# Kernel optimization log

Hardware: AMD Instinct MI355X
Metric: run time of the kernel (lower is better)

The kernel has to match this reference:

```python
import jax, jax.numpy as jnp
import numpy as np

N_HEADS = 16
D_MODEL = 1024
NEG_INF = float('-inf')


def _rope_tables(seq_len, d_k, dtype):
    # RoPE(dim=d_k//2): Theta_i = 10000^(-i/dim), repeat-interleaved to width d_k;
    # positions start at 1 (torch uses arange(1, max_len+1)).
    dim = d_k // 2
    theta = jnp.exp(-jnp.arange(dim, dtype=dtype) * (np.log(10000.0) / dim))
    theta = jnp.repeat(theta, 2)                      # [d_k]
    pos = jnp.arange(1, seq_len + 1, dtype=dtype)[:, None]  # [S,1]
    ang = pos * theta                                 # [S,d_k]
    return jnp.sin(ang), jnp.cos(ang)


def _rope(x):
    # x: [B,H,S,d_k]; pair rotation (x0,x1)->(-x1,x0), Rx = x*cos + rot(x)*sin
    B, H, S, d_k = x.shape
    sin, cos = _rope_tables(S, d_k, x.dtype)
    xp = x.reshape(B, H, S, d_k // 2, 2)
    rot = jnp.stack([-xp[..., 1], xp[..., 0]], axis=-1).reshape(x.shape)
    return x * cos + rot * sin


def setup_inputs() -> dict:
    key = jax.random.key(0)
    ks = jax.random.split(key, 8)
    B, S, D, H = 2, 1024, D_MODEL, N_HEADS
    source_query = jax.random.normal(ks[0], (B, S, D), dtype=jnp.float32)
    source_key_value = jax.random.normal(ks[1], (B, S, D), dtype=jnp.float32)
    # tail padding: lengths in [820, 1024]
    q_len = jax.random.randint(ks[2], (B,), 820, S + 1)
    kv_len = jax.random.randint(ks[3], (B,), 820, S + 1)
    pos = jnp.arange(S)
    source_query_padding_mask = pos[None, :] >= q_len[:, None]    # True = pad
    source_key_value_padding_mask = pos[None, :] >= kv_len[:, None]
    prev = jax.random.normal(ks[4], (1, B, H, S, S), dtype=jnp.float32) * 0.5
    Wq = jax.random.normal(ks[5], (D, D), dtype=jnp.float32) * 0.02
    Wk = jax.random.normal(ks[6], (D, D), dtype=jnp.float32) * 0.02
    kv2 = jax.random.split(ks[7], 2)
    Wv = jax.random.normal(kv2[0], (D, D), dtype=jnp.float32) * 0.02
    Wproj = jax.random.normal(kv2[1], (D, D), dtype=jnp.float32) * 0.02
    return dict(source_query=source_query, source_key_value=source_key_value,
                source_query_padding_mask=source_query_padding_mask,
                source_key_value_padding_mask=source_key_value_padding_mask,
                prev=prev, Wq=Wq, Wk=Wk, Wv=Wv, Wproj=Wproj)


def reference(source_query, source_key_value, source_query_padding_mask,
              source_key_value_padding_mask, prev, Wq, Wk, Wv, Wproj):
    B, Sq, D = source_query.shape
    Sk = source_key_value.shape[1]
    H = N_HEADS
    d_k = D // H

    def split_heads(x, S):
        return x.reshape(B, S, H, d_k).transpose(0, 2, 1, 3)  # [B,H,S,d_k]

    # nn.Linear(bias=False): y = x @ W.T
    q = split_heads(jnp.einsum('bsd,ed->bse', source_query, Wq), Sq)
    k = split_heads(jnp.einsum('bsd,ed->bse', source_key_value, Wk), Sk)
    v = split_heads(jnp.einsum('bsd,ed->bse', source_key_value, Wv), Sk)

    q = _rope(q)
    k = _rope(k)

    scores = jnp.einsum('bhqd,bhkd->bhqk', q, k) * (d_k ** -0.5)
    q_pad = source_query_padding_mask[:, None, :, None]   # [B,1,Sq,1]
    kv_pad = source_key_value_padding_mask[:, None, None, :]  # [B,1,1,Sk]
    scores = jnp.where(q_pad, NEG_INF, scores)
    scores = jnp.where(kv_pad, NEG_INF, scores)
    causal = jnp.tril(jnp.ones((Sq, Sq), dtype=bool))      # masked=True
    scores = jnp.where(causal, scores, NEG_INF)

    prev_new = jnp.concatenate([prev, scores[None]], axis=0)  # [L+1,B,H,Sq,Sk]
    avg = prev_new.mean(0)

    # rows fully -inf (padded queries) would softmax to NaN in torch, then get
    # filled with 0 -> compute a safe softmax and zero those rows instead.
    safe = jnp.where(q_pad, 0.0, avg)
    w = jax.nn.softmax(safe, axis=-1)
    w = jnp.where(q_pad, 0.0, w)

    attn = jnp.einsum('bhqk,bhkd->bhqd', w, v)
    attn = attn.transpose(0, 2, 1, 3).reshape(B, Sq, D)
    out = jnp.einsum('bsd,ed->bse', attn, Wproj)  # dropout=0 (eval)
    return out, prev_new
```

## Files before the change

kernel.cpp:

```cpp
#include <hip/hip_runtime.h>
#include <math.h>

#define NSEQ 1024
#define NH   16
#define DKH  64

#define NEGBIG (-1.0e30f)

__global__ __launch_bounds__(256) void normalize_masks(
    const unsigned char* __restrict__ qm, const unsigned char* __restrict__ km,
    int* __restrict__ outq, int* __restrict__ outk)
{
    __shared__ int flag;
    if (threadIdx.x == 0) flag = 0;
    __syncthreads();
    int f = 0;
    for (int i = threadIdx.x; i < 2048; i += 256) {
        if ((i & 3) && qm[i]) f = 1;
        if ((i & 3) && km[i]) f = 1;
    }
    if (f) atomicOr(&flag, 1);
    __syncthreads();
    const int isbyte = flag;
    for (int i = threadIdx.x; i < 2048; i += 256) {
        outq[i] = isbyte ? (int)qm[i] : ((const int*)qm)[i];
        outk[i] = isbyte ? (int)km[i] : ((const int*)km)[i];
    }
}

__device__ __forceinline__ void gemm_core(
    const float* __restrict__ X, const float* __restrict__ W,
    float (*As)[68], float (*Bs)[132], float (&acc)[8][4],
    int m0, int e0, int tid)
{
    const int tm = tid >> 5, tn = tid & 31;
    const int arow = tid >> 2, akq = (tid & 3) * 4;
    const int brow = tid >> 1, bkq = (tid & 1) * 8;
    const float* aptr = &X[(size_t)(m0 + arow) * 1024 + akq];
    const float* bptr = &W[(size_t)(e0 + brow) * 1024 + bkq];

    float4 ar  = *(const float4*)aptr;
    float4 br0 = *(const float4*)bptr;
    float4 br1 = *(const float4*)(bptr + 4);

    for (int k0 = 0; k0 < 1024; k0 += 16) {
        As[akq + 0][arow] = ar.x;  As[akq + 1][arow] = ar.y;
        As[akq + 2][arow] = ar.z;  As[akq + 3][arow] = ar.w;
        Bs[bkq + 0][brow] = br0.x; Bs[bkq + 1][brow] = br0.y;
        Bs[bkq + 2][brow] = br0.z; Bs[bkq + 3][brow] = br0.w;
        Bs[bkq + 4][brow] = br1.x; Bs[bkq + 5][brow] = br1.y;
        Bs[bkq + 6][brow] = br1.z; Bs[bkq + 7][brow] = br1.w;
        __syncthreads();
        if (k0 + 16 < 1024) {
            ar  = *(const float4*)(aptr + k0 + 16);
            br0 = *(const float4*)(bptr + k0 + 16);
            br1 = *(const float4*)(bptr + k0 + 16 + 4);
        }
        #pragma unroll
        for (int k = 0; k < 16; ++k) {
            float a[8], bb[4];
            *(float4*)&a[0]  = *(const float4*)&As[k][tm * 8];
            *(float4*)&a[4]  = *(const float4*)&As[k][tm * 8 + 4];
            *(float4*)&bb[0] = *(const float4*)&Bs[k][tn * 4];
            #pragma unroll
            for (int i = 0; i < 8; ++i)
                #pragma unroll
                for (int j = 0; j < 4; ++j)
                    acc[i][j] += a[i] * bb[j];
        }
        __syncthreads();
    }
}

__global__ __launch_bounds__(256) void gemm_qkv(
    const float* __restrict__ srcq, const float* __restrict__ srckv,
    const float* __restrict__ Wq, const float* __restrict__ Wk,
    const float* __restrict__ Wv,
    float* __restrict__ qh, float* __restrict__ kh, float* __restrict__ vh)
{
    __shared__ float As[16][68];
    __shared__ float Bs[16][132];
    const int tid = threadIdx.x;
    const int z = blockIdx.z;
    const float* X = (z == 0) ? srcq : srckv;
    const float* W = (z == 0) ? Wq : (z == 1) ? Wk : Wv;
    float* Y       = (z == 0) ? qh : (z == 1) ? kh : vh;
    const int m0 = blockIdx.y * 64, e0 = blockIdx.x * 128;

    float acc[8][4] = {{0.f}};
    gemm_core(X, W, As, Bs, acc, m0, e0, tid);

    const int tm = tid >> 5, tn = tid & 31;
    const int col = e0 + tn * 4;
    const int h = col >> 6, dbase = col & 63;
    const bool rope = (z != 2);
    float th0 = 0.f, th1 = 0.f;
    if (rope) {
        const float cth = 0.28782313662425575f;
        th0 = expf(-(float)(dbase >> 1) * cth);
        th1 = expf(-(float)((dbase >> 1) + 1) * cth);
    }
    #pragma unroll
    for (int i = 0; i < 8; ++i) {
        const int m = m0 + tm * 8 + i;
        const int b = m >> 10, s = m & 1023;
        float v0 = acc[i][0], v1 = acc[i][1], v2 = acc[i][2], v3 = acc[i][3];
        if (rope) {
            const float pos = (float)(s + 1);
            float s0, c0, s1, c1;
            sincosf(pos * th0, &s0, &c0);
            sincosf(pos * th1, &s1, &c1);
            float r0 = v0 * c0 - v1 * s0;
            float r1 = v1 * c0 + v0 * s0;
            float r2 = v2 * c1 - v3 * s1;
            float r3 = v3 * c1 + v2 * s1;
            v0 = r0; v1 = r1; v2 = r2; v3 = r3;
        }
        const size_t idx = (((size_t)(b * NH + h) << 10) + s) * DKH + dbase;
        *(float4*)&Y[idx] = make_float4(v0, v1, v2, v3);
    }
}

__global__ __launch_bounds__(256) void gemm_proj(
    const float* __restrict__ X, const float* __restrict__ W,
    float* __restrict__ Y)
{
    __shared__ float As[16][68];
    __shared__ float Bs[16][132];
    const int tid = threadIdx.x;
    const int m0 = blockIdx.y * 64, e0 = blockIdx.x * 128;
    float acc[8][4] = {{0.f}};
    gemm_core(X, W, As, Bs, acc, m0, e0, tid);
    const int tm = tid >> 5, tn = tid & 31;
    #pragma unroll
    for (int i = 0; i < 8; ++i)
        *(float4*)&Y[(size_t)(m0 + tm * 8 + i) * 1024 + e0 + tn * 4] =
            make_float4(acc[i][0], acc[i][1], acc[i][2], acc[i][3]);
}

__global__ __launch_bounds__(256) void flash_fused(
    const float* __restrict__ qh, const float* __restrict__ kh,
    const float* __restrict__ vh, const float* __restrict__ prev,
    const int* __restrict__ nmq, const int* __restrict__ nmk,
    float* __restrict__ prevc, float* __restrict__ scb,
    float* __restrict__ attn)
{
    const int bh = blockIdx.y;
    const int b = bh >> 4, h = bh & 15;
    const int bx = blockIdx.x;
    const int qt = (bx & 1) ? (15 - (bx >> 1)) : (bx >> 1);
    const int q0 = qt * 64;
    const int tid = threadIdx.x;
    const int ti = tid >> 4, tj = tid & 15;
    const int r0 = ti * 4, c0 = tj * 4;
    const size_t base = ((size_t)bh << 10) * 1024;
    const float NI = NEGBIG;

    __shared__ float Qs[64][68];
    __shared__ float KW[64][68];
    __shared__ float Vs[64][68];

    const int lr = tid >> 2;
    const int ld0 = (tid & 3) * 4;
    {
        const float* qbase = qh + (((size_t)bh << 10) + q0) * DKH;
        #pragma unroll
        for (int dq = 0; dq < 4; ++dq) {
            const int d0 = ld0 + dq * 16;
            float4 qv = *(const float4*)&qbase[(size_t)lr * DKH + d0];
            Qs[d0 + 0][lr] = qv.x; Qs[d0 + 1][lr] = qv.y;
            Qs[d0 + 2][lr] = qv.z; Qs[d0 + 3][lr] = qv.w;
        }
    }

    {
        const float4 ninf4 = make_float4(NI, NI, NI, NI);
        for (int kt = qt + 1; kt < 16; ++kt) {
            const int k0 = kt * 64;
            #pragma unroll
            for (int u = 0; u < 4; ++u) {
                const int e = u * 256 + tid;
                const int rr = e >> 4, cc = (e & 15) * 4;
                const size_t idx = base + (size_t)(q0 + rr) * 1024 + k0 + cc;
                *(float4*)&prevc[idx] = *(const float4*)&prev[idx];
                *(float4*)&scb[idx] = ninf4;
            }
        }
    }

    int qmv[4];
    #pragma unroll
    for (int i = 0; i < 4; ++i) qmv[i] = nmq[(b << 10) + q0 + r0 + i];

    float m_i[4], l_i[4], O[4][4];
    #pragma unroll
    for (int i = 0; i < 4; ++i) {
        m_i[i] = -3.0e38f; l_i[i] = 0.f;
        #pragma unroll
        for (int j = 0; j < 4; ++j) O[i][j] = 0.f;
    }

    const float* kbase = kh + ((size_t)bh << 10) * DKH;
    const float* vbase = vh + ((size_t)bh << 10) * DKH;

    for (int kt = 0; kt <= qt; ++kt) {
        const int k0 = kt * 64;
        __syncthreads();

        #pragma unroll
        for (int dq = 0; dq < 4; ++dq) {
            const int d0 = ld0 + dq * 16;
            float4 kv4 = *(const float4*)&kbase[(size_t)(k0 + lr) * DKH + d0];
            KW[d0 + 0][lr] = kv4.x; KW[d0 + 1][lr] = kv4.y;
            KW[d0 + 2][lr] = kv4.z; KW[d0 + 3][lr] = kv4.w;
        }
        #pragma unroll
        for (int u = 0; u < 4; ++u) {
            const int e = u * 256 + tid;
            const int kv = e >> 4, dd = (e & 15) * 4;
            *(float4*)&Vs[kv][dd] =
                *(const float4*)&vbase[(size_t)(k0 + kv) * DKH + dd];
        }
        __syncthreads();

        float acc[4][4] = {{0.f}};
        #pragma unroll 8
        for (int d = 0; d < 64; ++d) {
            float a[4], bb[4];
            *(float4*)a  = *(const float4*)&Qs[d][r0];
            *(float4*)bb = *(const float4*)&KW[d][c0];
            #pragma unroll
            for (int i = 0; i < 4; ++i)
                #pragma unroll
                for (int j = 0; j < 4; ++j)
                    acc[i][j] += a[i] * bb[j];
        }

        int km[4];
        #pragma unroll
        for (int j = 0; j < 4; ++j) km[j] = nmk[(b << 10) + k0 + c0 + j];
        float aw[4][4], tmx[4];
        #pragma unroll
        for (int i = 0; i < 4; ++i) {
            const int row = q0 + r0 + i;
            float o[4];
            #pragma unroll
            for (int j = 0; j < 4; ++j) {
                const int col = k0 + c0 + j;
                const bool masked = (col > row) || (qmv[i] != 0) || (km[j] != 0);
                o[j] = masked ? NI : acc[i][j] * 0.125f;
            }
            const size_t idx = base + (size_t)row * 1024 + k0 + c0;
            *(float4*)&scb[idx] = make_float4(o[0], o[1], o[2], o[3]);
            const float4 p4 = *(const float4*)&prev[idx];
            *(float4*)&prevc[idx] = p4;
            aw[i][0] = 0.5f * (p4.x + o[0]);
            aw[i][1] = 0.5f * (p4.y + o[1]);
            aw[i][2] = 0.5f * (p4.z + o[2]);
            aw[i][3] = 0.5f * (p4.w + o[3]);
            tmx[i] = fmaxf(fmaxf(aw[i][0], aw[i][1]), fmaxf(aw[i][2], aw[i][3]));
        }
        #pragma unroll
        for (int i = 0; i < 4; ++i)
            #pragma unroll
            for (int off = 1; off < 16; off <<= 1)
                tmx[i] = fmaxf(tmx[i], __shfl_xor(tmx[i], off));

        __syncthreads();

        #pragma unroll
        for (int i = 0; i < 4; ++i) {
            const float mn = fmaxf(m_i[i], tmx[i]);
            const float fac = expf(m_i[i] - mn);
            m_i[i] = mn;
            float w0 = expf(aw[i][0] - mn);
            float w1 = expf(aw[i][1] - mn);
            float w2 = expf(aw[i][2] - mn);
            float w3 = expf(aw[i][3] - mn);
            float sl = w0 + w1 + w2 + w3;
            #pragma unroll
            for (int off = 1; off < 16; off <<= 1)
                sl += __shfl_xor(sl, off);
            l_i[i] = l_i[i] * fac + sl;
            #pragma unroll
            for (int j = 0; j < 4; ++j) O[i][j] *= fac;
            KW[c0 + 0][r0 + i] = w0;
            KW[c0 + 1][r0 + i] = w1;
            KW[c0 + 2][r0 + i] = w2;
            KW[c0 + 3][r0 + i] = w3;
        }
        __syncthreads();

        #pragma unroll 8
        for (int k = 0; k < 64; ++k) {
            float wv[4], vv[4];
            *(float4*)wv = *(const float4*)&KW[k][r0];
            *(float4*)vv = *(const float4*)&Vs[k][c0];
            #pragma unroll
            for (int i = 0; i < 4; ++i)
                #pragma unroll
                for (int j = 0; j < 4; ++j)
                    O[i][j] += wv[i] * vv[j];
        }
    }

    #pragma unroll
    for (int i = 0; i < 4; ++i) {
        const int q = q0 + r0 + i;
        const float inv = qmv[i] ? 0.f : 1.f / l_i[i];
        float4 o4 = make_float4(O[i][0] * inv, O[i][1] * inv,
                                O[i][2] * inv, O[i][3] * inv);
        *(float4*)&attn[(size_t)((b << 10) + q) * 1024 + (h << 6) + c0] = o4;
    }
}

extern "C" void kernel_launch(void* const* d_in, const int* in_sizes, int n_in,
                              void* d_out, int out_size, void* d_ws, size_t ws_size,
                              hipStream_t stream) {
    const float* srcq  = (const float*)d_in[0];
    const float* srckv = (const float*)d_in[1];
    const void*  qmask = d_in[2];
    const void*  kmask = d_in[3];
    const float* prev  = (const float*)d_in[4];
    const float* Wq    = (const float*)d_in[5];
    const float* Wk    = (const float*)d_in[6];
    const float* Wv    = (const float*)d_in[7];
    const float* Wp    = (const float*)d_in[8];

    float* out0  = (float*)d_out;
    float* prevc = out0 + 2097152;
    float* scb   = prevc + 33554432;

    float* qh   = (float*)d_ws;
    float* kh   = qh + 2097152;
    float* vh   = kh + 2097152;
    float* attn = vh + 2097152;
    int*   nmq  = (int*)(attn + 2097152);
    int*   nmk  = nmq + 2048;

    hipLaunchKernelGGL(normalize_masks, dim3(1), dim3(256), 0, stream,
                       (const unsigned char*)qmask, (const unsigned char*)kmask, nmq, nmk);
    hipLaunchKernelGGL(gemm_qkv, dim3(8, 32, 3), dim3(256), 0, stream,
                       srcq, srckv, Wq, Wk, Wv, qh, kh, vh);
    hipLaunchKernelGGL(flash_fused, dim3(16, 32), dim3(256), 0, stream,
                       qh, kh, vh, prev, nmq, nmk, prevc, scb, attn);
    hipLaunchKernelGGL(gemm_proj, dim3(8, 32), dim3(256), 0, stream,
                       attn, Wp, out0);
}
```

Measured before the change: 727.2 us.

## Rework GEMM tiling, split upper-triangle copy, and warp-split flash attention

```diff
diff --git a/kernel.cpp b/kernel.cpp
--- a/kernel.cpp
+++ b/kernel.cpp
@@ -28,51 +28,65 @@
     }
 }
 
-__device__ __forceinline__ void gemm_core(
+__device__ __forceinline__ void gemm_core128(
     const float* __restrict__ X, const float* __restrict__ W,
-    float (*As)[68], float (*Bs)[132], float (&acc)[8][4],
+    float (*As)[68], float (*Bs)[132], float (&acc)[8][8],
     int m0, int e0, int tid)
 {
-    const int tm = tid >> 5, tn = tid & 31;
-    const int arow = tid >> 2, akq = (tid & 3) * 4;
-    const int brow = tid >> 1, bkq = (tid & 1) * 8;
+    const int r0 = (tid >> 4) * 8;
+    const int c0 = (tid & 15) * 8;
+    const int arow = tid >> 1, akq = (tid & 1) * 8;
+    const int brow = tid;
     const float* aptr = &X[(size_t)(m0 + arow) * 1024 + akq];
-    const float* bptr = &W[(size_t)(e0 + brow) * 1024 + bkq];
-
-    float4 ar  = *(const float4*)aptr;
+    const float* bptr = &W[(size_t)(e0 + brow) * 1024];
+
+    float4 ar0 = *(const float4*)aptr;
+    float4 ar1 = *(const float4*)(aptr + 4);
     float4 br0 = *(const float4*)bptr;
     float4 br1 = *(const float4*)(bptr + 4);
+    float4 br2 = *(const float4*)(bptr + 8);
+    float4 br3 = *(const float4*)(bptr + 12);
 
     for (int k0 = 0; k0 < 1024; k0 += 16) {
-        As[akq + 0][arow] = ar.x;  As[akq + 1][arow] = ar.y;
-        As[akq + 2][arow] = ar.z;  As[akq + 3][arow] = ar.w;
-        Bs[bkq + 0][brow] = br0.x; Bs[bkq + 1][brow] = br0.y;
-        Bs[bkq + 2][brow] = br0.z; Bs[bkq + 3][brow] = br0.w;
-        Bs[bkq + 4][brow] = br1.x; Bs[bkq + 5][brow] = br1.y;
-        Bs[bkq + 6][brow] = br1.z; Bs[bkq + 7][brow] = br1.w;
+        As[akq + 0][arow] = ar0.x; As[akq + 1][arow] = ar0.y;
+        As[akq + 2][arow] = ar0.z; As[akq + 3][arow] = ar0.w;
+        As[akq + 4][arow] = ar1.x; As[akq + 5][arow] = ar1.y;
+        As[akq + 6][arow] = ar1.z; As[akq + 7][arow] = ar1.w;
+        Bs[ 0][brow] = br0.x; Bs[ 1][brow] = br0.y;
+        Bs[ 2][brow] = br0.z; Bs[ 3][brow] = br0.w;
+        Bs[ 4][brow] = br1.x; Bs[ 5][brow] = br1.y;
+        Bs[ 6][brow] = br1.z; Bs[ 7][brow] = br1.w;
+        Bs[ 8][brow] = br2.x; Bs[ 9][brow] = br2.y;
+        Bs[10][brow] = br2.z; Bs[11][brow] = br2.w;
+        Bs[12][brow] = br3.x; Bs[13][brow] = br3.y;
+        Bs[14][brow] = br3.z; Bs[15][brow] = br3.w;
         __syncthreads();
         if (k0 + 16 < 1024) {
-            ar  = *(const float4*)(aptr + k0 + 16);
+            ar0 = *(const float4*)(aptr + k0 + 16);
+            ar1 = *(const float4*)(aptr + k0 + 20);
             br0 = *(const float4*)(bptr + k0 + 16);
-            br1 = *(const float4*)(bptr + k0 + 16 + 4);
+            br1 = *(const float4*)(bptr + k0 + 20);
+            br2 = *(const float4*)(bptr + k0 + 24);
+            br3 = *(const float4*)(bptr + k0 + 28);
         }
         #pragma unroll
         for (int k = 0; k < 16; ++k) {
-            float a[8], bb[4];
-            *(float4*)&a[0]  = *(const float4*)&As[k][tm * 8];
-            *(float4*)&a[4]  = *(const float4*)&As[k][tm * 8 + 4];
-            *(float4*)&bb[0] = *(const float4*)&Bs[k][tn * 4];
+            float a[8], bb[8];
+            *(float4*)&a[0]  = *(const float4*)&As[k][r0];
+            *(float4*)&a[4]  = *(const float4*)&As[k][r0 + 4];
+            *(float4*)&bb[0] = *(const float4*)&Bs[k][c0];
+            *(float4*)&bb[4] = *(const float4*)&Bs[k][c0 + 4];
             #pragma unroll
             for (int i = 0; i < 8; ++i)
                 #pragma unroll
-                for (int j = 0; j < 4; ++j)
+                for (int j = 0; j < 8; ++j)
                     acc[i][j] += a[i] * bb[j];
         }
         __syncthreads();
     }
 }
 
-__global__ __launch_bounds__(256) void gemm_qkv(
+__global__ __launch_bounds__(128) void gemm_qkv(
     const float* __restrict__ srcq, const float* __restrict__ srckv,
     const float* __restrict__ Wq, const float* __restrict__ Wk,
     const float* __restrict__ Wv,
@@ -87,41 +101,46 @@
     float* Y       = (z == 0) ? qh : (z == 1) ? kh : vh;
     const int m0 = blockIdx.y * 64, e0 = blockIdx.x * 128;
 
-    float acc[8][4] = {{0.f}};
-    gemm_core(X, W, As, Bs, acc, m0, e0, tid);
-
-    const int tm = tid >> 5, tn = tid & 31;
-    const int col = e0 + tn * 4;
+    float acc[8][8] = {{0.f}};
+    gemm_core128(X, W, As, Bs, acc, m0, e0, tid);
+
+    const int r0 = (tid >> 4) * 8;
+    const int c0 = (tid & 15) * 8;
+    const int col = e0 + c0;
     const int h = col >> 6, dbase = col & 63;
     const bool rope = (z != 2);
-    float th0 = 0.f, th1 = 0.f;
+    float th[4];
     if (rope) {
         const float cth = 0.28782313662425575f;
-        th0 = expf(-(float)(dbase >> 1) * cth);
-        th1 = expf(-(float)((dbase >> 1) + 1) * cth);
+        #pragma unroll
+        for (int p = 0; p < 4; ++p)
+            th[p] = expf(-(float)((dbase >> 1) + p) * cth);
     }
     #pragma unroll
     for (int i = 0; i < 8; ++i) {
-        const int m = m0 + tm * 8 + i;
+        const int m = m0 + r0 + i;
         const int b = m >> 10, s = m & 1023;
-        float v0 = acc[i][0], v1 = acc[i][1], v2 = acc[i][2], v3 = acc[i][3];
+        float v[8];
+        #pragma unroll
+        for (int j = 0; j < 8; ++j) v[j] = acc[i][j];
         if (rope) {
             const float pos = (float)(s + 1);
-            float s0, c0, s1, c1;
-            sincosf(pos * th0, &s0, &c0);
-            sincosf(pos * th1, &s1, &c1);
-            float r0 = v0 * c0 - v1 * s0;
-            float r1 = v1 * c0 + v0 * s0;
-            float r2 = v2 * c1 - v3 * s1;
-            float r3 = v3 * c1 + v2 * s1;
-            v0 = r0; v1 = r1; v2 = r2; v3 = r3;
+            #pragma unroll
+            for (int p = 0; p < 4; ++p) {
+                float sp, cp;
+                sincosf(pos * th[p], &sp, &cp);
+                const float ve = v[2 * p], vo = v[2 * p + 1];
+                v[2 * p]     = ve * cp - vo * sp;
+                v[2 * p + 1] = vo * cp + ve * sp;
+            }
         }
         const size_t idx = (((size_t)(b * NH + h) << 10) + s) * DKH + dbase;
-        *(float4*)&Y[idx] = make_float4(v0, v1, v2, v3);
-    }
-}
-
-__global__ __launch_bounds__(256) void gemm_proj(
+        *(float4*)&Y[idx]     = make_float4(v[0], v[1], v[2], v[3]);
+        *(float4*)&Y[idx + 4] = make_float4(v[4], v[5], v[6], v[7]);
+    }
+}
+
+__global__ __launch_bounds__(128) void gemm_proj(
     const float* __restrict__ X, const float* __restrict__ W,
     float* __restrict__ Y)
 {
@@ -129,16 +148,36 @@
     __shared__ float Bs[16][132];
     const int tid = threadIdx.x;
     const int m0 = blockIdx.y * 64, e0 = blockIdx.x * 128;
-    float acc[8][4] = {{0.f}};
-    gemm_core(X, W, As, Bs, acc, m0, e0, tid);
-    const int tm = tid >> 5, tn = tid & 31;
-    #pragma unroll
-    for (int i = 0; i < 8; ++i)
-        *(float4*)&Y[(size_t)(m0 + tm * 8 + i) * 1024 + e0 + tn * 4] =
-            make_float4(acc[i][0], acc[i][1], acc[i][2], acc[i][3]);
-}
-
-__global__ __launch_bounds__(256) void flash_fused(
+    float acc[8][8] = {{0.f}};
+    gemm_core128(X, W, As, Bs, acc, m0, e0, tid);
+    const int r0 = (tid >> 4) * 8;
+    const int c0 = (tid & 15) * 8;
+    #pragma unroll
+    for (int i = 0; i < 8; ++i) {
+        const size_t idx = (size_t)(m0 + r0 + i) * 1024 + e0 + c0;
+        *(float4*)&Y[idx]     = make_float4(acc[i][0], acc[i][1], acc[i][2], acc[i][3]);
+        *(float4*)&Y[idx + 4] = make_float4(acc[i][4], acc[i][5], acc[i][6], acc[i][7]);
+    }
+}
+
+__global__ __launch_bounds__(256) void upper_copy(
+    const float* __restrict__ prev, float* __restrict__ prevc,
+    float* __restrict__ scb)
+{
+    const int kt = blockIdx.x, qt = blockIdx.y, bh = blockIdx.z;
+    if (kt <= qt) return;
+    const size_t base = ((size_t)bh << 10) * 1024;
+    const int row = threadIdx.x >> 2, ch = (threadIdx.x & 3) * 16;
+    const float4 n4 = make_float4(NEGBIG, NEGBIG, NEGBIG, NEGBIG);
+    const size_t idx = base + (size_t)(qt * 64 + row) * 1024 + kt * 64 + ch;
+    #pragma unroll
+    for (int c = 0; c < 4; ++c) {
+        *(float4*)&prevc[idx + c * 4] = *(const float4*)&prev[idx + c * 4];
+        *(float4*)&scb[idx + c * 4]   = n4;
+    }
+}
+
+__global__ __launch_bounds__(256, 2) void flash_fused(
     const float* __restrict__ qh, const float* __restrict__ kh,
     const float* __restrict__ vh, const float* __restrict__ prev,
     const int* __restrict__ nmq, const int* __restrict__ nmk,
@@ -151,166 +190,161 @@
     const int qt = (bx & 1) ? (15 - (bx >> 1)) : (bx >> 1);
     const int q0 = qt * 64;
     const int tid = threadIdx.x;
-    const int ti = tid >> 4, tj = tid & 15;
-    const int r0 = ti * 4, c0 = tj * 4;
+    const int wid = tid >> 6, lane = tid & 63;
+    const int ri = lane >> 3, cj = lane & 7;
+    const int c0 = cj * 8;
     const size_t base = ((size_t)bh << 10) * 1024;
-    const float NI = NEGBIG;
 
     __shared__ float Qs[64][68];
-    __shared__ float KW[64][68];
-    __shared__ float Vs[64][68];
-
-    const int lr = tid >> 2;
-    const int ld0 = (tid & 3) * 4;
+
     {
         const float* qbase = qh + (((size_t)bh << 10) + q0) * DKH;
-        #pragma unroll
-        for (int dq = 0; dq < 4; ++dq) {
-            const int d0 = ld0 + dq * 16;
-            float4 qv = *(const float4*)&qbase[(size_t)lr * DKH + d0];
-            Qs[d0 + 0][lr] = qv.x; Qs[d0 + 1][lr] = qv.y;
-            Qs[d0 + 2][lr] = qv.z; Qs[d0 + 3][lr] = qv.w;
-        }
-    }
-
-    {
-        const float4 ninf4 = make_float4(NI, NI, NI, NI);
-        for (int kt = qt + 1; kt < 16; ++kt) {
-            const int k0 = kt * 64;
-            #pragma unroll
-            for (int u = 0; u < 4; ++u) {
-                const int e = u * 256 + tid;
-                const int rr = e >> 4, cc = (e & 15) * 4;
-                const size_t idx = base + (size_t)(q0 + rr) * 1024 + k0 + cc;
-                *(float4*)&prevc[idx] = *(const float4*)&prev[idx];
-                *(float4*)&scb[idx] = ninf4;
-            }
-        }
-    }
-
-    int qmv[4];
-    #pragma unroll
-    for (int i = 0; i < 4; ++i) qmv[i] = nmq[(b << 10) + q0 + r0 + i];
-
-    float m_i[4], l_i[4], O[4][4];
-    #pragma unroll
-    for (int i = 0; i < 4; ++i) {
+        const int row = tid >> 2, ch = (tid & 3) * 16;
+        #pragma unroll
+        for (int c = 0; c < 4; ++c)
+            *(float4*)&Qs[row][ch + c * 4] =
+                *(const float4*)&qbase[(size_t)row * DKH + ch + c * 4];
+    }
+    __syncthreads();
+
+    int qmv[8];
+    #pragma unroll
+    for (int i = 0; i < 8; ++i) qmv[i] = nmq[(b << 10) + q0 + ri + 8 * i];
+
+    float S[8][8], O[8][8], m_i[8], l_i[8];
+    #pragma unroll
+    for (int i = 0; i < 8; ++i) {
         m_i[i] = -3.0e38f; l_i[i] = 0.f;
         #pragma unroll
-        for (int j = 0; j < 4; ++j) O[i][j] = 0.f;
+        for (int j = 0; j < 8; ++j) O[i][j] = 0.f;
     }
 
     const float* kbase = kh + ((size_t)bh << 10) * DKH;
     const float* vbase = vh + ((size_t)bh << 10) * DKH;
 
-    for (int kt = 0; kt <= qt; ++kt) {
+    for (int kt = wid; kt <= qt; kt += 4) {
         const int k0 = kt * 64;
-        __syncthreads();
-
-        #pragma unroll
-        for (int dq = 0; dq < 4; ++dq) {
-            const int d0 = ld0 + dq * 16;
-            float4 kv4 = *(const float4*)&kbase[(size_t)(k0 + lr) * DKH + d0];
-            KW[d0 + 0][lr] = kv4.x; KW[d0 + 1][lr] = kv4.y;
-            KW[d0 + 2][lr] = kv4.z; KW[d0 + 3][lr] = kv4.w;
-        }
-        #pragma unroll
-        for (int u = 0; u < 4; ++u) {
-            const int e = u * 256 + tid;
-            const int kv = e >> 4, dd = (e & 15) * 4;
-            *(float4*)&Vs[kv][dd] =
-                *(const float4*)&vbase[(size_t)(k0 + kv) * DKH + dd];
-        }
-        __syncthreads();
-
-        float acc[4][4] = {{0.f}};
-        #pragma unroll 8
-        for (int d = 0; d < 64; ++d) {
-            float a[4], bb[4];
-            *(float4*)a  = *(const float4*)&Qs[d][r0];
-            *(float4*)bb = *(const float4*)&KW[d][c0];
-            #pragma unroll
-            for (int i = 0; i < 4; ++i)
+
+        #pragma unroll
+        for (int i = 0; i < 8; ++i)
+            #pragma unroll
+            for (int j = 0; j < 8; ++j) S[i][j] = 0.f;
+        #pragma unroll 2
+        for (int d0 = 0; d0 < 64; d0 += 4) {
+            float4 kv[8];
+            #pragma unroll
+            for (int j = 0; j < 8; ++j)
+                kv[j] = *(const float4*)&kbase[(size_t)(k0 + c0 + j) * DKH + d0];
+            #pragma unroll
+            for (int i = 0; i < 8; ++i) {
+                const float4 qv = *(const float4*)&Qs[ri + 8 * i][d0];
                 #pragma unroll
-                for (int j = 0; j < 4; ++j)
-                    acc[i][j] += a[i] * bb[j];
-        }
-
-        int km[4];
-        #pragma unroll
-        for (int j = 0; j < 4; ++j) km[j] = nmk[(b << 10) + k0 + c0 + j];
-        float aw[4][4], tmx[4];
-        #pragma unroll
-        for (int i = 0; i < 4; ++i) {
-            const int row = q0 + r0 + i;
-            float o[4];
-            #pragma unroll
-            for (int j = 0; j < 4; ++j) {
+                for (int j = 0; j < 8; ++j)
+                    S[i][j] += qv.x * kv[j].x + qv.y * kv[j].y +
+                               qv.z * kv[j].z + qv.w * kv[j].w;
+            }
+        }
+
+        int km[8];
+        #pragma unroll
+        for (int j = 0; j < 8; ++j) km[j] = nmk[(b << 10) + k0 + c0 + j];
+        #pragma unroll
+        for (int i = 0; i < 8; ++i) {
+            const int row = q0 + ri + 8 * i;
+            float o[8];
+            #pragma unroll
+            for (int j = 0; j < 8; ++j) {
                 const int col = k0 + c0 + j;
                 const bool masked = (col > row) || (qmv[i] != 0) || (km[j] != 0);
-                o[j] = masked ? NI : acc[i][j] * 0.125f;
+                o[j] = masked ? NEGBIG : S[i][j] * 0.125f;
             }
             const size_t idx = base + (size_t)row * 1024 + k0 + c0;
-            *(float4*)&scb[idx] = make_float4(o[0], o[1], o[2], o[3]);
-            const float4 p4 = *(const float4*)&prev[idx];
-            *(float4*)&prevc[idx] = p4;
-            aw[i][0] = 0.5f * (p4.x + o[0]);
-            aw[i][1] = 0.5f * (p4.y + o[1]);
-            aw[i][2] = 0.5f * (p4.z + o[2]);
-            aw[i][3] = 0.5f * (p4.w + o[3]);
-            tmx[i] = fmaxf(fmaxf(aw[i][0], aw[i][1]), fmaxf(aw[i][2], aw[i][3]));
-        }
-        #pragma unroll
-        for (int i = 0; i < 4; ++i)
-            #pragma unroll
-            for (int off = 1; off < 16; off <<= 1)
-                tmx[i] = fmaxf(tmx[i], __shfl_xor(tmx[i], off));
-
-        __syncthreads();
-
-        #pragma unroll
-        for (int i = 0; i < 4; ++i) {
-            const float mn = fmaxf(m_i[i], tmx[i]);
+            *(float4*)&scb[idx]     = make_float4(o[0], o[1], o[2], o[3]);
+            *(float4*)&scb[idx + 4] = make_float4(o[4], o[5], o[6], o[7]);
+            const float4 p0 = *(const float4*)&prev[idx];
+            const float4 p1 = *(const float4*)&prev[idx + 4];
+            *(float4*)&prevc[idx]     = p0;
+            *(float4*)&prevc[idx + 4] = p1;
+            S[i][0] = 0.5f * (p0.x + o[0]); S[i][1] = 0.5f * (p0.y + o[1]);
+            S[i][2] = 0.5f * (p0.z + o[2]); S[i][3] = 0.5f * (p0.w + o[3]);
+            S[i][4] = 0.5f * (p1.x + o[4]); S[i][5] = 0.5f * (p1.y + o[5]);
+            S[i][6] = 0.5f * (p1.z + o[6]); S[i][7] = 0.5f * (p1.w + o[7]);
+        }
+
+        #pragma unroll
+        for (int i = 0; i < 8; ++i) {
+            float t = fmaxf(fmaxf(fmaxf(S[i][0], S[i][1]), fmaxf(S[i][2], S[i][3])),
+                            fmaxf(fmaxf(S[i][4], S[i][5]), fmaxf(S[i][6], S[i][7])));
+            t = fmaxf(t, __shfl_xor(t, 1));
+            t = fmaxf(t, __shfl_xor(t, 2));
+            t = fmaxf(t, __shfl_xor(t, 4));
+            const float mn = fmaxf(m_i[i], t);
             const float fac = expf(m_i[i] - mn);
             m_i[i] = mn;
-            float w0 = expf(aw[i][0] - mn);
-            float w1 = expf(aw[i][1] - mn);
-            float w2 = expf(aw[i][2] - mn);
-            float w3 = expf(aw[i][3] - mn);
-            float sl = w0 + w1 + w2 + w3;
-            #pragma unroll
-            for (int off = 1; off < 16; off <<= 1)
-                sl += __shfl_xor(sl, off);
+            float sl = 0.f;
+            #pragma unroll
+            for (int j = 0; j < 8; ++j) { S[i][j] = expf(S[i][j] - mn); sl += S[i][j]; }
+            sl += __shfl_xor(sl, 1);
+            sl += __shfl_xor(sl, 2);
+            sl += __shfl_xor(sl, 4);
             l_i[i] = l_i[i] * fac + sl;
             #pragma unroll
-            for (int j = 0; j < 4; ++j) O[i][j] *= fac;
-            KW[c0 + 0][r0 + i] = w0;
-            KW[c0 + 1][r0 + i] = w1;
-            KW[c0 + 2][r0 + i] = w2;
-            KW[c0 + 3][r0 + i] = w3;
+            for (int j = 0; j < 8; ++j) O[i][j] *= fac;
+        }
+
+        for (int kc = 0; kc < 8; ++kc) {
+            #pragma unroll
+            for (int kj = 0; kj < 8; ++kj) {
+                const int k = k0 + kc * 8 + kj;
+                const float4 v0 = *(const float4*)&vbase[(size_t)k * DKH + c0];
+                const float4 v1 = *(const float4*)&vbase[(size_t)k * DKH + c0 + 4];
+                #pragma unroll
+                for (int i = 0; i < 8; ++i) {
+                    const float w = __shfl(S[i][kj], ri * 8 + kc);
+                    O[i][0] += w * v0.x; O[i][1] += w * v0.y;
+                    O[i][2] += w * v0.z; O[i][3] += w * v0.w;
+                    O[i][4] += w * v1.x; O[i][5] += w * v1.y;
+                    O[i][6] += w * v1.z; O[i][7] += w * v1.w;
+                }
+            }
+        }
+    }
+
+    __syncthreads();
+    for (int w = 0; w < 4; ++w) {
+        if (wid == w) {
+            #pragma unroll
+            for (int i = 0; i < 8; ++i) {
+                const int row = ri + 8 * i;
+                if (w == 0) {
+                    #pragma unroll
+                    for (int j = 0; j < 8; ++j) Qs[row][c0 + j] = O[i][j];
+                    if (cj == 0) { Qs[row][64] = m_i[i]; Qs[row][65] = l_i[i]; }
+                } else {
+                    const float Mold = Qs[row][64], Lold = Qs[row][65];
+                    const float mn = fmaxf(Mold, m_i[i]);
+                    const float fo = expf(Mold - mn), fw = expf(m_i[i] - mn);
+                    #pragma unroll
+                    for (int j = 0; j < 8; ++j)
+                        Qs[row][c0 + j] = Qs[row][c0 + j] * fo + O[i][j] * fw;
+                    if (cj == 0) { Qs[row][64] = mn; Qs[row][65] = Lold * fo + l_i[i] * fw; }
+                }
+            }
         }
         __syncthreads();
-
-        #pragma unroll 8
-        for (int k = 0; k < 64; ++k) {
-            float wv[4], vv[4];
-            *(float4*)wv = *(const float4*)&KW[k][r0];
-            *(float4*)vv = *(const float4*)&Vs[k][c0];
-            #pragma unroll
-            for (int i = 0; i < 4; ++i)
-                #pragma unroll
-                for (int j = 0; j < 4; ++j)
-                    O[i][j] += wv[i] * vv[j];
-        }
-    }
-
-    #pragma unroll
-    for (int i = 0; i < 4; ++i) {
-        const int q = q0 + r0 + i;
-        const float inv = qmv[i] ? 0.f : 1.f / l_i[i];
-        float4 o4 = make_float4(O[i][0] * inv, O[i][1] * inv,
-                                O[i][2] * inv, O[i][3] * inv);
-        *(float4*)&attn[(size_t)((b << 10) + q) * 1024 + (h << 6) + c0] = o4;
+    }
+
+    {
+        const int row = tid >> 2, ch = (tid & 3) * 16;
+        const int qp = nmq[(b << 10) + q0 + row];
+        const float L = Qs[row][65];
+        const float inv = qp ? 0.f : 1.f / L;
+        #pragma unroll
+        for (int c = 0; c < 4; ++c) {
+            float4 v = *(const float4*)&Qs[row][ch + c * 4];
+            v.x *= inv; v.y *= inv; v.z *= inv; v.w *= inv;
+            *(float4*)&attn[(size_t)((b << 10) + q0 + row) * 1024 + (h << 6) + ch + c * 4] = v;
+        }
     }
 }
 
@@ -340,10 +374,12 @@
 
     hipLaunchKernelGGL(normalize_masks, dim3(1), dim3(256), 0, stream,
                        (const unsigned char*)qmask, (const unsigned char*)kmask, nmq, nmk);
-    hipLaunchKernelGGL(gemm_qkv, dim3(8, 32, 3), dim3(256), 0, stream,
+    hipLaunchKernelGGL(gemm_qkv, dim3(8, 32, 3), dim3(128), 0, stream,
                        srcq, srckv, Wq, Wk, Wv, qh, kh, vh);
+    hipLaunchKernelGGL(upper_copy, dim3(16, 16, 32), dim3(256), 0, stream,
+                       prev, prevc, scb);
     hipLaunchKernelGGL(flash_fused, dim3(16, 32), dim3(256), 0, stream,
                        qh, kh, vh, prev, nmq, nmk, prevc, scb, attn);
-    hipLaunchKernelGGL(gemm_proj, dim3(8, 32), dim3(256), 0, stream,
+    hipLaunchKernelGGL(gemm_proj, dim3(8, 32), dim3(128), 0, stream,
                        attn, Wp, out0);
 }
```

Measured after the change: 997.7 us. +37.2%, slower.
